# Kernel tuning notes

Measured on AMD Instinct MI355X. Metric: run time of the kernel, lower is better.

Reference implementation:

```python
import jax, jax.numpy as jnp
import numpy as np

D_MODEL = 768
N_HEADS = 12
D_FF = 3072
EPS = 1e-5


def _layernorm(x, g, b):
    mu = jnp.mean(x, axis=-1, keepdims=True)
    var = jnp.mean(jnp.square(x - mu), axis=-1, keepdims=True)
    return (x - mu) * jax.lax.rsqrt(var + EPS) * g + b


def setup_inputs() -> dict:
    key = jax.random.key(0)
    ks = jax.random.split(key, 16)
    d, f = D_MODEL, D_FF
    s = 1.0 / np.sqrt(d)
    inp = {
        "x": jax.random.normal(ks[0], (1, 4096, d), dtype=jnp.float32),
        "Wq": jax.random.normal(ks[1], (d, d), dtype=jnp.float32) * s,
        "bq": jnp.zeros((d,), jnp.float32),
        "Wk": jax.random.normal(ks[2], (d, d), dtype=jnp.float32) * s,
        "bk": jnp.zeros((d,), jnp.float32),
        "Wv": jax.random.normal(ks[3], (d, d), dtype=jnp.float32) * s,
        "bv": jnp.zeros((d,), jnp.float32),
        "Wo": jax.random.normal(ks[4], (d, d), dtype=jnp.float32) * s,
        "bo": jnp.zeros((d,), jnp.float32),
        "ln1_g": jnp.ones((d,), jnp.float32),
        "ln1_b": jnp.zeros((d,), jnp.float32),
        "ln2_g": jnp.ones((d,), jnp.float32),
        "ln2_b": jnp.zeros((d,), jnp.float32),
        "W1": jax.random.normal(ks[5], (d, f), dtype=jnp.float32) * s,
        "b1": jnp.zeros((f,), jnp.float32),
        "W2": jax.random.normal(ks[6], (f, d), dtype=jnp.float32) * (1.0 / np.sqrt(f)),
        "b2": jnp.zeros((d,), jnp.float32),
    }
    return inp


def reference(x, Wq, bq, Wk, bk, Wv, bv, Wo, bo, ln1_g, ln1_b, ln2_g, ln2_b, W1, b1, W2, b2):
    b, s, d = x.shape
    h = N_HEADS
    dk = d // h

    # --- attention sublayer (pre-norm residual) ---
    xn = _layernorm(x, ln1_g, ln1_b)

    def proj(W, bias):
        y = xn @ W + bias                      # [b, s, d]
        return y.reshape(b, s, h, dk).transpose(0, 2, 1, 3)  # [b, h, s, dk]

    q, k, v = proj(Wq, bq), proj(Wk, bk), proj(Wv, bv)
    scores = jnp.einsum("bhqd,bhkd->bhqk", q, k) / np.sqrt(dk)
    attn = jax.nn.softmax(scores, axis=-1)
    ctx = jnp.einsum("bhqk,bhkd->bhqd", attn, v)
    ctx = ctx.transpose(0, 2, 1, 3).reshape(b, s, d)
    x = x + (ctx @ Wo + bo)

    # --- FFN sublayer (pre-norm residual) ---
    xn2 = _layernorm(x, ln2_g, ln2_b)
    ff = jax.nn.gelu(xn2 @ W1 + b1, approximate=False) @ W2 + b2
    return x + ff
```

## Files before the change

### kernel.cpp

```cpp
#include <hip/hip_runtime.h>
#include <hip/hip_bf16.h>

typedef __attribute__((ext_vector_type(8))) __bf16 bf16x8;
typedef __attribute__((ext_vector_type(4))) __bf16 bf16x4;
typedef __attribute__((ext_vector_type(4))) float f32x4;
typedef __attribute__((ext_vector_type(4))) unsigned short u16x4;
typedef unsigned short ushort_t;

__device__ __forceinline__ ushort_t f2bf(float f) {
    union { float f; unsigned u; } v; v.f = f;
    unsigned r = v.u + 0x7fffu + ((v.u >> 16) & 1u);
    return (ushort_t)(r >> 16);
}

__device__ __forceinline__ void gload16(const ushort_t* g, ushort_t* l) {
    __builtin_amdgcn_global_load_lds(
        (const __attribute__((address_space(1))) unsigned int*)g,
        (__attribute__((address_space(3))) unsigned int*)l,
        16, 0, 0);
}

__device__ __forceinline__ void ln_row(const float* __restrict__ xr,
                                       const float* __restrict__ g,
                                       const float* __restrict__ b,
                                       ushort_t* __restrict__ orow, int t) {
    float v0 = xr[t], v1 = xr[t + 256], v2 = xr[t + 512];
    float s  = v0 + v1 + v2;
    float s2 = v0 * v0 + v1 * v1 + v2 * v2;
#pragma unroll
    for (int off = 32; off; off >>= 1) {
        s  += __shfl_down(s, off);
        s2 += __shfl_down(s2, off);
    }
    __shared__ float red[8];
    const int wid = t >> 6, lane = t & 63;
    if (lane == 0) { red[wid] = s; red[4 + wid] = s2; }
    __syncthreads();
    __shared__ float stats[2];
    if (t == 0) {
        float S = red[0] + red[1] + red[2] + red[3];
        float S2 = red[4] + red[5] + red[6] + red[7];
        float mu = S * (1.0f / 768.0f);
        float var = S2 * (1.0f / 768.0f) - mu * mu;
        stats[0] = mu;
        stats[1] = rsqrtf(var + 1e-5f);
    }
    __syncthreads();
    const float mu = stats[0], rs = stats[1];
    orow[t]       = f2bf((v0 - mu) * rs * g[t]       + b[t]);
    orow[t + 256] = f2bf((v1 - mu) * rs * g[t + 256] + b[t + 256]);
    orow[t + 512] = f2bf((v2 - mu) * rs * g[t + 512] + b[t + 512]);
}

__global__ __launch_bounds__(256) void ln_kernel(const float* __restrict__ x,
                                                 const float* __restrict__ g,
                                                 const float* __restrict__ b,
                                                 ushort_t* __restrict__ out) {
    const int row = blockIdx.x;
    ln_row(x + (size_t)row * 768, g, b, out + (size_t)row * 768, threadIdx.x);
}

__global__ __launch_bounds__(256) void prep_ln(
    const float* __restrict__ Wq, const float* __restrict__ Wk,
    const float* __restrict__ Wv, const float* __restrict__ Wo,
    const float* __restrict__ W1, const float* __restrict__ W2,
    const float* __restrict__ bq, const float* __restrict__ bk,
    const float* __restrict__ bv,
    const float* __restrict__ x, const float* __restrict__ ln1_g,
    const float* __restrict__ ln1_b,
    ushort_t* __restrict__ WqkvT, ushort_t* __restrict__ WoT,
    ushort_t* __restrict__ W1T, ushort_t* __restrict__ W2T,
    float* __restrict__ bqkv, ushort_t* __restrict__ xn) {
    const int bid = blockIdx.x;
    const int t = threadIdx.x;
    if (bid >= 6915) {
        const int row = bid - 6915;
        ln_row(x + (size_t)row * 768, ln1_g, ln1_b, xn + (size_t)row * 768, t);
        return;
    }
    if (bid >= 6912) {
        const int i = bid - 6912;
        const float* s = (i == 0) ? bq : (i == 1) ? bk : bv;
#pragma unroll
        for (int j = t; j < 768; j += 256) bqkv[i * 768 + j] = s[j];
        return;
    }
    const float* src; ushort_t* dst; int R, C, ti;
    if (bid < 576)       { src = Wq; dst = WqkvT;               R = 768;  C = 768;  ti = bid; }
    else if (bid < 1152) { src = Wk; dst = WqkvT + 768 * 768;   R = 768;  C = 768;  ti = bid - 576; }
    else if (bid < 1728) { src = Wv; dst = WqkvT + 2 * 768 * 768; R = 768; C = 768; ti = bid - 1152; }
    else if (bid < 2304) { src = Wo; dst = WoT;                 R = 768;  C = 768;  ti = bid - 1728; }
    else if (bid < 4608) { src = W1; dst = W1T;                 R = 768;  C = 3072; ti = bid - 2304; }
    else                 { src = W2; dst = W2T;                 R = 3072; C = 768;  ti = bid - 4608; }
    const int tpr = C >> 5;
    const int c0 = (ti % tpr) * 32, r0 = (ti / tpr) * 32;
    __shared__ float tile[32][33];
    {
        const int c = t & 31, r = t >> 5;
#pragma unroll
        for (int i = 0; i < 4; i++)
            tile[r + i * 8][c] = src[(size_t)(r0 + r + i * 8) * C + c0 + c];
    }
    __syncthreads();
    {
        const int oc = t >> 3, q = t & 7;
        u16x4 o;
#pragma unroll
        for (int k = 0; k < 4; k++) o[k] = f2bf(tile[q * 4 + k][oc]);
        *(u16x4*)&dst[(size_t)(c0 + oc) * R + r0 + q * 4] = o;
    }
}

template <int BN, int GELU, int RES, int OUTF, int OUTB, int OUTV>
__global__ __launch_bounds__(256, 3)
void gemm_bt(const ushort_t* __restrict__ A, const ushort_t* __restrict__ Bt,
             const float* __restrict__ bias, const float* __restrict__ res,
             float* __restrict__ outF, ushort_t* __restrict__ outB, int ldo,
             ushort_t* __restrict__ outV,
             int M, int N, int K) {
    constexpr int TR  = 128 + BN;
    constexpr int LL  = TR / 64;
    constexpr int WCF = BN / 32;
    __shared__ __align__(16) ushort_t Ls[2][TR * 32];

    const int nbx = gridDim.x;
    const int nwg = nbx * gridDim.y;
    int fb = blockIdx.y * nbx + blockIdx.x;
    fb = (fb & 7) * (nwg >> 3) + (fb >> 3);
    const int m0 = (fb / nbx) * 128, n0 = (fb % nbx) * BN;

    const int t = threadIdx.x;
    const int wid = t >> 6, lane = t & 63;
    const int wr = wid >> 1, wc = wid & 1;
    const int row16 = lane & 15, kg = lane >> 4;
    const int kb = kg * 8;

    const int srow = lane >> 2, scol = (lane & 3) * 8;
    const ushort_t* gsrc[LL];
    int lofs[LL];
#pragma unroll
    for (int i = 0; i < LL; i++) {
        const int r0 = wid * (TR / 4) + 16 * i;
        gsrc[i] = (r0 < 128 ? A + (size_t)(m0 + r0 + srow) * K
                            : Bt + (size_t)(n0 + r0 - 128 + srow) * K) + scol;
        lofs[i] = r0 * 32;
    }

#define STAGE(buf, kofs) do {                                        \
        _Pragma("unroll")                                            \
        for (int i = 0; i < LL; i++)                                 \
            gload16(gsrc[i] + (kofs), &Ls[buf][lofs[i]]);            \
    } while (0)

    f32x4 acc[4][WCF] = {};
    const int NS = K >> 5;
    STAGE(0, 0);
    STAGE(1, 32);
    int cur = 0;

    for (int s = 0; s < NS; ++s) {
        if (s + 1 == NS) asm volatile("s_waitcnt vmcnt(0)" ::: "memory");
        else             asm volatile("s_waitcnt vmcnt(%0)" :: "i"(LL) : "memory");
        __builtin_amdgcn_s_barrier();

        bf16x8 a[4], b[WCF];
#pragma unroll
        for (int i = 0; i < 4; i++)
            a[i] = *(const bf16x8*)&Ls[cur][(wr * 64 + i * 16 + row16) * 32 + kb];
#pragma unroll
        for (int j = 0; j < WCF; j++)
            b[j] = *(const bf16x8*)&Ls[cur][(128 + wc * (BN / 2) + j * 16 + row16) * 32 + kb];
        asm volatile("s_waitcnt lgkmcnt(0)" ::: "memory");
        __builtin_amdgcn_s_barrier();
        if (s + 2 < NS) STAGE(cur, (s + 2) * 32);

        __builtin_amdgcn_s_setprio(1);
#pragma unroll
        for (int i = 0; i < 4; i++)
#pragma unroll
            for (int j = 0; j < WCF; j++)
                acc[i][j] = __builtin_amdgcn_mfma_f32_16x16x32_bf16(a[i], b[j], acc[i][j], 0, 0, 0);
        __builtin_amdgcn_s_setprio(0);
        cur ^= 1;
    }
#undef STAGE

#pragma unroll
    for (int i = 0; i < 4; i++)
#pragma unroll
        for (int j = 0; j < WCF; j++) {
            const int col = n0 + wc * (BN / 2) + j * 16 + row16;
            const float bv = bias[col];
            const int rb = m0 + wr * 64 + i * 16 + kg * 4;
            if (OUTV && col >= 1536) {
                bf16x4 pk;
#pragma unroll
                for (int r = 0; r < 4; r++) pk[r] = (__bf16)(acc[i][j][r] + bv);
                *(bf16x4*)&outV[(size_t)(col - 1536) * 4096 + rb] = pk;
            } else {
#pragma unroll
                for (int r = 0; r < 4; r++) {
                    const int row = rb + r;
                    float v = acc[i][j][r] + bv;
                    if (GELU) {
                        float u = v + 0.044715f * v * v * v;
                        float e = __builtin_amdgcn_exp2f(2.30220779f * u);
                        v = v * e * __builtin_amdgcn_rcpf(e + 1.0f);
                    }
                    if (RES) v += res[(size_t)row * N + col];
                    if (OUTF) outF[(size_t)row * N + col] = v;
                    if (OUTB) outB[(size_t)row * ldo + col] = f2bf(v);
                }
            }
        }
}

__device__ __forceinline__ int swz(int row, int col) {
    return row * 64 + (col ^ ((row & 7) << 3));
}

__global__ __launch_bounds__(256, 2)
void attn_kernel(const ushort_t* __restrict__ qk,
                 const ushort_t* __restrict__ Vt,
                 ushort_t* __restrict__ ctx) {
    int fb = blockIdx.y * 32 + blockIdx.x;
    fb = (fb & 7) * 48 + (fb >> 3);
    const int q0 = (fb & 31) * 128;
    const int h  = fb >> 5;

    const int t  = threadIdx.x;
    const int w = t >> 6, lane = t & 63;
    const int row16 = lane & 15, kg = lane >> 4;
    const int kb = kg * 8;

    __shared__ __align__(16) ushort_t Ps[128 * 64];
    __shared__ __align__(16) ushort_t Ks[2][64 * 64];
    __shared__ __align__(16) ushort_t Vs[2][64 * 64];

    {
        const int qr = t >> 1, cb = (t & 1) * 32;
        const size_t qbase = (size_t)(q0 + qr) * 1536 + h * 64 + cb;
#pragma unroll
        for (int j = 0; j < 4; j++)
            *(uint4*)&Ps[swz(qr, cb + j * 8)] = *(const uint4*)&qk[qbase + j * 8];
    }
    {
        const int sr = t >> 2, sc = (t & 3) * 8;
        const size_t kbase = (size_t)sr * 1536 + 768 + h * 64 + sc;
        *(uint4*)&Ks[0][swz(sr, sc)]      = *(const uint4*)&qk[kbase];
        *(uint4*)&Ks[0][swz(sr, sc + 32)] = *(const uint4*)&qk[kbase + 32];
        const size_t vbase = (size_t)(h * 64 + sr) * 4096 + sc;
        *(uint4*)&Vs[0][swz(sr, sc)]      = *(const uint4*)&Vt[vbase];
        *(uint4*)&Vs[0][swz(sr, sc + 32)] = *(const uint4*)&Vt[vbase + 32];
    }
    bf16x8 qa0[2], qa1[2];
#pragma unroll
    for (int qb = 0; qb < 2; qb++) {
        qa0[qb] = *(const bf16x8*)&Ps[swz(w * 32 + qb * 16 + row16, kb)];
        qa1[qb] = *(const bf16x8*)&Ps[swz(w * 32 + qb * 16 + row16, 32 + kb)];
    }
    __syncthreads();

    const int rr = lane >> 3;
    const int gcol = ((lane & 7) ^ rr) * 8;
    const ushort_t* gK = qk + 768 + h * 64 + gcol + (size_t)(w * 16 + rr) * 1536;
    const ushort_t* gV = Vt + (size_t)(h * 64 + w * 16 + rr) * 4096 + gcol;

    bf16x8 vones;
#pragma unroll
    for (int i = 0; i < 8; i++) vones[i] = (__bf16)1.0f;

    f32x4 o_acc[2][4] = {};
    f32x4 o_l[2] = {};
    int cur = 0;
    const float SC = 0.18033688011112042f;

    for (int it = 0; it < 64; ++it) {
        if (it != 63) {
            const int kv1 = (it + 1) * 64;
            ushort_t* kd = &Ks[cur ^ 1][w * 1024];
            ushort_t* vd = &Vs[cur ^ 1][w * 1024];
            gload16(gK + (size_t)kv1 * 1536,       kd);
            gload16(gK + (size_t)(kv1 + 8) * 1536, kd + 512);
            gload16(gV + kv1,                      vd);
            gload16(gV + kv1 + 8 * 4096,           vd + 512);
        }

        const ushort_t* Kc = Ks[cur];
        const ushort_t* Vc = Vs[cur];

        bf16x8 ka0[4], ka1[4];
#pragma unroll
        for (int f = 0; f < 4; f++) {
            ka0[f] = *(const bf16x8*)&Kc[swz(f * 16 + row16, kb)];
            ka1[f] = *(const bf16x8*)&Kc[swz(f * 16 + row16, 32 + kb)];
        }

        f32x4 s_acc[2][4];
        __builtin_amdgcn_s_setprio(1);
#pragma unroll
        for (int qb = 0; qb < 2; qb++)
#pragma unroll
            for (int f = 0; f < 4; f++) {
                f32x4 z = {};
                z = __builtin_amdgcn_mfma_f32_16x16x32_bf16(ka0[f], qa0[qb], z, 0, 0, 0);
                s_acc[qb][f] = __builtin_amdgcn_mfma_f32_16x16x32_bf16(ka1[f], qa1[qb], z, 0, 0, 0);
            }
        __builtin_amdgcn_s_setprio(0);

#pragma unroll
        for (int qb = 0; qb < 2; qb++)
#pragma unroll
            for (int f = 0; f < 4; f++) {
                bf16x4 pk;
#pragma unroll
                for (int r = 0; r < 4; r++)
                    pk[r] = (__bf16)__builtin_amdgcn_exp2f(fminf(s_acc[qb][f][r] * SC, 30.0f));
                *(bf16x4*)&Ps[swz(w * 32 + qb * 16 + row16, f * 16 + kg * 4)] = pk;
            }

        bf16x8 pa0[2], pa1[2];
#pragma unroll
        for (int qb = 0; qb < 2; qb++) {
            pa0[qb] = *(const bf16x8*)&Ps[swz(w * 32 + qb * 16 + row16, kb)];
            pa1[qb] = *(const bf16x8*)&Ps[swz(w * 32 + qb * 16 + row16, 32 + kb)];
        }
        __builtin_amdgcn_s_setprio(1);
#pragma unroll
        for (int f = 0; f < 4; f++) {
            bf16x8 vb0 = *(const bf16x8*)&Vc[swz(f * 16 + row16, kb)];
            bf16x8 vb1 = *(const bf16x8*)&Vc[swz(f * 16 + row16, 32 + kb)];
#pragma unroll
            for (int qb = 0; qb < 2; qb++) {
                o_acc[qb][f] = __builtin_amdgcn_mfma_f32_16x16x32_bf16(pa0[qb], vb0, o_acc[qb][f], 0, 0, 0);
                o_acc[qb][f] = __builtin_amdgcn_mfma_f32_16x16x32_bf16(pa1[qb], vb1, o_acc[qb][f], 0, 0, 0);
            }
        }
#pragma unroll
        for (int qb = 0; qb < 2; qb++) {
            o_l[qb] = __builtin_amdgcn_mfma_f32_16x16x32_bf16(pa0[qb], vones, o_l[qb], 0, 0, 0);
            o_l[qb] = __builtin_amdgcn_mfma_f32_16x16x32_bf16(pa1[qb], vones, o_l[qb], 0, 0, 0);
        }
        __builtin_amdgcn_s_setprio(0);

        __syncthreads();
        cur ^= 1;
    }

#pragma unroll
    for (int qb = 0; qb < 2; qb++)
#pragma unroll
        for (int f = 0; f < 4; f++)
#pragma unroll
            for (int r = 0; r < 4; r++) {
                const int qrow = q0 + w * 32 + qb * 16 + kg * 4 + r;
                ctx[(size_t)qrow * 768 + h * 64 + f * 16 + row16] =
                    f2bf(o_acc[qb][f][r] / o_l[qb][r]);
            }
}

extern "C" void kernel_launch(void* const* d_in, const int* in_sizes, int n_in,
                              void* d_out, int out_size, void* d_ws, size_t ws_size,
                              hipStream_t stream) {
    const float* x     = (const float*)d_in[0];
    const float* Wq    = (const float*)d_in[1];
    const float* bq    = (const float*)d_in[2];
    const float* Wk    = (const float*)d_in[3];
    const float* bk    = (const float*)d_in[4];
    const float* Wv    = (const float*)d_in[5];
    const float* bv    = (const float*)d_in[6];
    const float* Wo    = (const float*)d_in[7];
    const float* bo    = (const float*)d_in[8];
    const float* ln1_g = (const float*)d_in[9];
    const float* ln1_b = (const float*)d_in[10];
    const float* ln2_g = (const float*)d_in[11];
    const float* ln2_b = (const float*)d_in[12];
    const float* W1    = (const float*)d_in[13];
    const float* b1    = (const float*)d_in[14];
    const float* W2    = (const float*)d_in[15];
    const float* b2    = (const float*)d_in[16];

    char* ws = (char*)d_ws;
    ushort_t* WqkvT = (ushort_t*)ws; ws += (size_t)2304 * 768 * 2;
    ushort_t* WoT   = (ushort_t*)ws; ws += (size_t)768 * 768 * 2;
    ushort_t* W1T   = (ushort_t*)ws; ws += (size_t)3072 * 768 * 2;
    ushort_t* W2T   = (ushort_t*)ws; ws += (size_t)768 * 3072 * 2;
    float*    bqkv  = (float*)ws;    ws += (size_t)2304 * 4;
    ushort_t* xn    = (ushort_t*)ws; ws += (size_t)4096 * 768 * 2;
    ushort_t* qk    = (ushort_t*)ws; ws += (size_t)4096 * 1536 * 2;
    ushort_t* Vtb   = (ushort_t*)ws; ws += (size_t)768 * 4096 * 2;
    ushort_t* ctxb  = (ushort_t*)ws; ws += (size_t)4096 * 768 * 2;
    float*    x1    = (float*)ws;    ws += (size_t)4096 * 768 * 4;
    ushort_t* H     = qk;

    prep_ln<<<6915 + 4096, 256, 0, stream>>>(Wq, Wk, Wv, Wo, W1, W2, bq, bk, bv,
                                             x, ln1_g, ln1_b,
                                             WqkvT, WoT, W1T, W2T, bqkv, xn);

    gemm_bt<128, 0, 0, 0, 1, 1><<<dim3(18, 32), 256, 0, stream>>>(
        xn, WqkvT, bqkv, nullptr, nullptr, qk, 1536, Vtb, 4096, 2304, 768);

    attn_kernel<<<dim3(32, 12), 256, 0, stream>>>(qk, Vtb, ctxb);

    gemm_bt<64, 0, 1, 1, 0, 0><<<dim3(12, 32), 256, 0, stream>>>(
        ctxb, WoT, bo, x, x1, nullptr, 0, nullptr, 4096, 768, 768);

    ln_kernel<<<4096, 256, 0, stream>>>(x1, ln2_g, ln2_b, xn);
    gemm_bt<128, 1, 0, 0, 1, 0><<<dim3(24, 32), 256, 0, stream>>>(
        xn, W1T, b1, nullptr, nullptr, H, 3072, nullptr, 4096, 3072, 768);
    gemm_bt<64, 0, 1, 1, 0, 0><<<dim3(12, 32), 256, 0, stream>>>(
        H, W2T, b2, x1, (float*)d_out, nullptr, 0, nullptr, 4096, 768, 3072);

    (void)in_sizes; (void)n_in; (void)out_size; (void)ws_size;
}
```

Measured before the change: 222.5 us.

## Split attention KV range across two blocks and add a combine kernel

The attention kernel now splits each head's 4096 keys into two halves. The grid doubles to 768 blocks, with launch bounds raised to 3 blocks per CU, to fill the GPU more evenly. Each half writes unnormalized fp32 numerators and row denominators to workspace (one buffer aliases x1). A new elementwise kernel sums the halves, normalizes and packs to bf16. The trade-off is extra fp32 global traffic, one more launch, and possible register pressure from the higher occupancy target.

New measurement: 201.3 us. 9.5% less time.

```diff
diff --git a/kernel.cpp b/kernel.cpp
--- a/kernel.cpp
+++ b/kernel.cpp
@@ -219,14 +219,17 @@
     return row * 64 + (col ^ ((row & 7) << 3));
 }
 
-__global__ __launch_bounds__(256, 2)
+__global__ __launch_bounds__(256, 3)
 void attn_kernel(const ushort_t* __restrict__ qk,
                  const ushort_t* __restrict__ Vt,
-                 ushort_t* __restrict__ ctx) {
+                 float* __restrict__ num0, float* __restrict__ num1,
+                 float* __restrict__ den) {
     int fb = blockIdx.y * 32 + blockIdx.x;
-    fb = (fb & 7) * 48 + (fb >> 3);
+    fb = (fb & 7) * 96 + (fb >> 3);
     const int q0 = (fb & 31) * 128;
-    const int h  = fb >> 5;
+    const int hs = fb >> 5;
+    const int h = hs >> 1, sp = hs & 1;
+    const int kt0 = sp * 32;
 
     const int t  = threadIdx.x;
     const int w = t >> 6, lane = t & 63;
@@ -246,10 +249,10 @@
     }
     {
         const int sr = t >> 2, sc = (t & 3) * 8;
-        const size_t kbase = (size_t)sr * 1536 + 768 + h * 64 + sc;
+        const size_t kbase = (size_t)(kt0 * 64 + sr) * 1536 + 768 + h * 64 + sc;
         *(uint4*)&Ks[0][swz(sr, sc)]      = *(const uint4*)&qk[kbase];
         *(uint4*)&Ks[0][swz(sr, sc + 32)] = *(const uint4*)&qk[kbase + 32];
-        const size_t vbase = (size_t)(h * 64 + sr) * 4096 + sc;
+        const size_t vbase = (size_t)(h * 64 + sr) * 4096 + kt0 * 64 + sc;
         *(uint4*)&Vs[0][swz(sr, sc)]      = *(const uint4*)&Vt[vbase];
         *(uint4*)&Vs[0][swz(sr, sc + 32)] = *(const uint4*)&Vt[vbase + 32];
     }
@@ -275,9 +278,9 @@
     int cur = 0;
     const float SC = 0.18033688011112042f;
 
-    for (int it = 0; it < 64; ++it) {
-        if (it != 63) {
-            const int kv1 = (it + 1) * 64;
+    for (int it = 0; it < 32; ++it) {
+        if (it != 31) {
+            const int kv1 = (kt0 + it + 1) * 64;
             ushort_t* kd = &Ks[cur ^ 1][w * 1024];
             ushort_t* vd = &Vs[cur ^ 1][w * 1024];
             gload16(gK + (size_t)kv1 * 1536,       kd);
@@ -347,6 +350,7 @@
         cur ^= 1;
     }
 
+    float* np = sp ? num1 : num0;
 #pragma unroll
     for (int qb = 0; qb < 2; qb++)
 #pragma unroll
@@ -354,9 +358,39 @@
 #pragma unroll
             for (int r = 0; r < 4; r++) {
                 const int qrow = q0 + w * 32 + qb * 16 + kg * 4 + r;
-                ctx[(size_t)qrow * 768 + h * 64 + f * 16 + row16] =
-                    f2bf(o_acc[qb][f][r] / o_l[qb][r]);
-            }
+                np[(size_t)qrow * 768 + h * 64 + f * 16 + row16] = o_acc[qb][f][r];
+            }
+    if (row16 == 0 && h == 0) {
+    }
+    if (row16 == 0) {
+#pragma unroll
+        for (int qb = 0; qb < 2; qb++)
+#pragma unroll
+            for (int r = 0; r < 4; r++) {
+                const int qrow = q0 + w * 32 + qb * 16 + kg * 4 + r;
+                den[((size_t)sp * 12 + h) * 4096 + qrow] = o_l[qb][r];
+            }
+    }
+}
+
+__global__ __launch_bounds__(256) void attn_combine(
+    const float* __restrict__ num0, const float* __restrict__ num1,
+    const float* __restrict__ den, ushort_t* __restrict__ ctx) {
+    const int idx = blockIdx.x * 256 + threadIdx.x;
+    const int q = idx / 192;
+    const int g = idx % 192;
+    const int h = g >> 4;
+    const float rd = __builtin_amdgcn_rcpf(den[(size_t)h * 4096 + q] +
+                                           den[((size_t)12 + h) * 4096 + q]);
+    const size_t o = (size_t)q * 768 + g * 4;
+    float4 a = *(const float4*)&num0[o];
+    float4 b = *(const float4*)&num1[o];
+    u16x4 pk;
+    pk[0] = f2bf((a.x + b.x) * rd);
+    pk[1] = f2bf((a.y + b.y) * rd);
+    pk[2] = f2bf((a.z + b.z) * rd);
+    pk[3] = f2bf((a.w + b.w) * rd);
+    *(u16x4*)&ctx[o] = pk;
 }
 
 extern "C" void kernel_launch(void* const* d_in, const int* in_sizes, int n_in,
@@ -391,7 +425,10 @@
     ushort_t* Vtb   = (ushort_t*)ws; ws += (size_t)768 * 4096 * 2;
     ushort_t* ctxb  = (ushort_t*)ws; ws += (size_t)4096 * 768 * 2;
     float*    x1    = (float*)ws;    ws += (size_t)4096 * 768 * 4;
+    float*    num1  = (float*)ws;    ws += (size_t)4096 * 768 * 4;
+    float*    den   = (float*)ws;    ws += (size_t)2 * 12 * 4096 * 4;
     ushort_t* H     = qk;
+    float*    num0  = x1;
 
     prep_ln<<<6915 + 4096, 256, 0, stream>>>(Wq, Wk, Wv, Wo, W1, W2, bq, bk, bv,
                                              x, ln1_g, ln1_b,
@@ -400,7 +437,8 @@
     gemm_bt<128, 0, 0, 0, 1, 1><<<dim3(18, 32), 256, 0, stream>>>(
         xn, WqkvT, bqkv, nullptr, nullptr, qk, 1536, Vtb, 4096, 2304, 768);
 
-    attn_kernel<<<dim3(32, 12), 256, 0, stream>>>(qk, Vtb, ctxb);
+    attn_kernel<<<dim3(32, 24), 256, 0, stream>>>(qk, Vtb, num0, num1, den);
+    attn_combine<<<3072, 256, 0, stream>>>(num0, num1, den, ctxb);
 
     gemm_bt<64, 0, 1, 1, 0, 0><<<dim3(12, 32), 256, 0, stream>>>(
         ctxb, WoT, bo, x, x1, nullptr, 0, nullptr, 4096, 768, 768);
```
